# Kernel tuning notes

Hardware: AMD Instinct MI355X
Metric: run time of the kernel (lower is better)

The kernel has to match this reference:

```python
import jax, jax.numpy as jnp
import numpy as np

WD, WH, WW = 7, 7, 7  # 3D window size


def _relative_position_index():
    # Matches the torch buffer construction exactly.
    coords = np.stack(np.meshgrid(np.arange(WD), np.arange(WH), np.arange(WW), indexing='ij'))  # [3,wd,wh,ww]
    cf = coords.reshape(3, -1)                      # [3, n]
    rel = cf[:, :, None] - cf[:, None, :]           # [3, n, n]
    rel = rel.transpose(1, 2, 0).copy()             # [n, n, 3]
    rel[..., 0] += WD - 1
    rel[..., 1] += WH - 1
    rel[..., 2] += WW - 1
    rel[..., 0] *= (2 * WH - 1) * (2 * WW - 1)
    rel[..., 1] *= (2 * WW - 1)
    return rel.sum(-1).astype(np.int32)             # [n, n] in [0, 2197)


def setup_inputs() -> dict:
    key = jax.random.key(0)
    ks = jax.random.split(key, 10)
    DIM, H = 192, 6
    B, N, NW = 256, WD * WH * WW, 64  # b = batch*num_windows, NW divides B
    TABLE = (2 * WD - 1) * (2 * WH - 1) * (2 * WW - 1)  # 2197
    w_std = 0.02
    mask = jnp.where(jax.random.uniform(ks[2], (NW, N, N)) < 0.1, -100.0, 0.0).astype(jnp.float32)
    return {
        'x_q': jax.random.normal(ks[0], (B, N, DIM), jnp.float32),
        'x_kv': jax.random.normal(ks[1], (B, N, DIM), jnp.float32),
        'mask': mask,
        'q_w': jax.random.normal(ks[3], (DIM, DIM), jnp.float32) * w_std,
        'q_b': jnp.zeros((DIM,), jnp.float32),
        'kv_w': jax.random.normal(ks[4], (2 * DIM, DIM), jnp.float32) * w_std,
        'kv_b': jnp.zeros((2 * DIM,), jnp.float32),
        'proj_w': jax.random.normal(ks[5], (DIM, DIM), jnp.float32) * w_std,
        'proj_b': jnp.zeros((DIM,), jnp.float32),
        'rpb_table': jax.random.normal(ks[6], (TABLE, H), jnp.float32) * w_std,
        'rpi': jnp.asarray(_relative_position_index()),
    }


def reference(x_q, x_kv, mask, q_w, q_b, kv_w, kv_b, proj_w, proj_b, rpb_table, rpi):
    b, n, c = x_q.shape
    h = rpb_table.shape[-1]
    d = c // h
    scale = d ** (-0.5)
    # projections (torch Linear: y = x @ W.T + b)
    q = (x_q @ q_w.T + q_b).reshape(b, n, h, d)
    kv = x_kv @ kv_w.T + kv_b                      # [b, n, 2c]
    k = kv[..., :c].reshape(b, n, h, d)
    v = kv[..., c:].reshape(b, n, h, d)
    # windowed QK^T
    attn = jnp.einsum('bnhd,bmhd->bhnm', q * scale, k)  # [b, h, n, n]
    # gathered relative-position bias
    rpb = rpb_table[rpi[:n, :n].reshape(-1)].reshape(n, n, h).transpose(2, 0, 1)  # [h, n, n]
    attn = attn + rpb[None]
    # window mask add
    nw = mask.shape[0]
    attn = attn.reshape(b // nw, nw, h, n, n) + mask[None, :, None]
    attn = jax.nn.softmax(attn.reshape(b, h, n, n), axis=-1)
    out = jnp.einsum('bhnm,bmhd->bnhd', attn, v).reshape(b, n, c)
    return out @ proj_w.T + proj_b
```

## Files before the change

### kernel.cpp

```cpp
#include <hip/hip_runtime.h>
#include <hip/hip_bf16.h>
#include <cstdint>

#define B_    256
#define N_    343
#define C_    192
#define H_    6
#define D_    32
#define NW_   64
#define M_    (B_*N_)
#define NN_   (N_*N_)
#define VTS_  352
#define VLS_  360
#define RPG_  86
#define SCALE_ 0.17677669529663687f
#define LOG2E_ 1.4426950408889634f
#define SCALE_LOG2E_ (SCALE_ * LOG2E_)

typedef unsigned short ushort_t;
typedef __attribute__((ext_vector_type(8))) short short8;
typedef __attribute__((ext_vector_type(4))) float f32x4;
typedef __attribute__((ext_vector_type(16))) float f32x16;

__device__ __forceinline__ float b2f(unsigned int u) {
    return __uint_as_float(u << 16);
}
__device__ __forceinline__ unsigned int f2b(float f) {
    unsigned int x = __float_as_uint(f);
    x += 0x7FFFu + ((x >> 16) & 1u);
    return x >> 16;
}
__device__ __forceinline__ unsigned int cvt_pk(float a, float b) {
    unsigned int r;
    asm("v_cvt_pk_bf16_f32 %0, %1, %2" : "=v"(r) : "v"(a), "v"(b));
    return r;
}
__device__ __forceinline__ void pswap(unsigned int &x, unsigned int &y) {
    asm("v_permlane32_swap_b32 %0, %1" : "+v"(x), "+v"(y));
}

__global__ __launch_bounds__(256) void wcvt(
    const float* __restrict__ qw, const float* __restrict__ kvw,
    const float* __restrict__ pw, ushort_t* __restrict__ wb)
{
    int i = blockIdx.x * 256 + threadIdx.x;
    if (i >= 36864) return;
    float4 v;
    if (i < 9216)       v = ((const float4*)qw)[i];
    else if (i < 27648) v = ((const float4*)kvw)[i - 9216];
    else                v = ((const float4*)pw)[i - 27648];
    uint2 u;
    u.x = cvt_pk(v.x, v.y);
    u.y = cvt_pk(v.z, v.w);
    ((uint2*)wb)[i] = u;
}

__global__ __launch_bounds__(512, 4) void gemm_qkv(
    const float* __restrict__ xq, const float* __restrict__ xkv,
    const ushort_t* __restrict__ wb,
    const float* __restrict__ qbias, const float* __restrict__ kvbias,
    ushort_t* __restrict__ qx, ushort_t* __restrict__ kx,
    ushort_t* __restrict__ vtb)
{
    __shared__ ushort_t wls[192 * 200];

    const int t = threadIdx.x, wv = t >> 6, lane = t & 63;
    const int quad = lane >> 4, col = lane & 15;
    const int lid = blockIdx.x;
    const int xcd = lid & 7, idx = lid >> 3;
    const int wg = (xcd < 2 ? xcd * 258 : 2 * 258 + (xcd - 2) * 257) + idx;
    const int jsel = wg % 3;
    const int m0 = (wg / 3) * 128;
    const ushort_t* W = wb + (size_t)jsel * 36864;
    const float* Xf = (jsel == 0) ? xq : xkv;
    const float* bias = (jsel == 0) ? qbias : (jsel == 1 ? kvbias : kvbias + 192);
    const float alpha = (jsel == 0) ? SCALE_LOG2E_ : 1.0f;

    float4 a0[6], a1[6];
    {
        const float* xp = Xf + (size_t)(m0 + wv * 16 + col) * 192;
        #pragma unroll
        for (int kt = 0; kt < 6; ++kt) {
            a0[kt] = *(const float4*)(xp + kt * 32 + quad * 8);
            a1[kt] = *(const float4*)(xp + kt * 32 + quad * 8 + 4);
        }
    }

    for (int c = t; c < 4608; c += 512) {
        int row = c / 24, off = (c % 24) * 8;
        *(short8*)(wls + row * 200 + off) = *(const short8*)(W + row * 192 + off);
    }

    short8 xf[6];
    #pragma unroll
    for (int kt = 0; kt < 6; ++kt) {
        union { short8 s; unsigned int u[4]; } f;
        f.u[0] = cvt_pk(a0[kt].x, a0[kt].y);
        f.u[1] = cvt_pk(a0[kt].z, a0[kt].w);
        f.u[2] = cvt_pk(a1[kt].x, a1[kt].y);
        f.u[3] = cvt_pk(a1[kt].z, a1[kt].w);
        xf[kt] = f.s;
    }
    __syncthreads();

    f32x4 acc[12] = {};
    #pragma unroll
    for (int kt = 0; kt < 6; ++kt)
        #pragma unroll
        for (int ct = 0; ct < 12; ++ct) {
            short8 wf = *(const short8*)(wls + (ct * 16 + col) * 200 + kt * 32 + quad * 8);
            acc[ct] = __builtin_amdgcn_mfma_f32_16x16x32_bf16(wf, xf[kt], acc[ct], 0, 0, 0);
        }

    if (jsel < 2) {
        ushort_t* o16 = (jsel == 0) ? qx : kx;
        int m = m0 + wv * 16 + col;
        int bb = m / N_, nn = m - bb * N_;
        #pragma unroll
        for (int ct = 0; ct < 12; ++ct) {
            float4 bv = *(const float4*)(bias + ct * 16 + quad * 4);
            int hh = ct >> 1;
            int dbase = (ct & 1) * 16 + quad * 4;
            float v0 = (acc[ct][0] + bv.x) * alpha;
            float v1 = (acc[ct][1] + bv.y) * alpha;
            float v2 = (acc[ct][2] + bv.z) * alpha;
            float v3 = (acc[ct][3] + bv.w) * alpha;
            uint2 pk;
            pk.x = cvt_pk(v0, v1);
            pk.y = cvt_pk(v2, v3);
            *(uint2*)(o16 + (((size_t)bb * H_ + hh) * N_ + nn) * D_ + dbase) = pk;
        }
    } else {
        int m = m0 + wv * 16 + col;
        int bb = m / N_, nn = m - bb * N_;
        #pragma unroll
        for (int ct = 0; ct < 12; ++ct) {
            float4 bv = *(const float4*)(bias + ct * 16 + quad * 4);
            int hh = ct >> 1;
            int d0 = (ct & 1) * 16 + quad * 4;
            unsigned int u01 = cvt_pk(acc[ct][0] + bv.x, acc[ct][1] + bv.y);
            unsigned int u23 = cvt_pk(acc[ct][2] + bv.z, acc[ct][3] + bv.w);
            ushort_t* vp = vtb + (((size_t)bb * H_ + hh) * D_ + d0) * VTS_ + nn;
            vp[0]            = (ushort_t)u01;
            vp[VTS_]         = (ushort_t)(u01 >> 16);
            vp[2 * VTS_]     = (ushort_t)u23;
            vp[3 * VTS_]     = (ushort_t)(u23 >> 16);
        }
    }
}

__global__ __launch_bounds__(512, 4) void gemm_out(
    const ushort_t* __restrict__ aob, const ushort_t* __restrict__ wb,
    const float* __restrict__ pbias, float* __restrict__ out)
{
    __shared__ ushort_t wls[192 * 200];

    const int t = threadIdx.x, wv = t >> 6, lane = t & 63;
    const int quad = lane >> 4, col = lane & 15;
    const int m0 = blockIdx.x * 128;
    const ushort_t* W = wb + (size_t)3 * 36864;

    short8 xf[6];
    {
        const ushort_t* xp = aob + (size_t)(m0 + wv * 16 + col) * 192;
        #pragma unroll
        for (int kt = 0; kt < 6; ++kt)
            xf[kt] = *(const short8*)(xp + kt * 32 + quad * 8);
    }
    for (int c = t; c < 4608; c += 512) {
        int row = c / 24, off = (c % 24) * 8;
        *(short8*)(wls + row * 200 + off) = *(const short8*)(W + row * 192 + off);
    }
    __syncthreads();

    f32x4 acc[12] = {};
    #pragma unroll
    for (int kt = 0; kt < 6; ++kt)
        #pragma unroll
        for (int ct = 0; ct < 12; ++ct) {
            short8 wf = *(const short8*)(wls + (ct * 16 + col) * 200 + kt * 32 + quad * 8);
            acc[ct] = __builtin_amdgcn_mfma_f32_16x16x32_bf16(wf, xf[kt], acc[ct], 0, 0, 0);
        }

    int m = m0 + wv * 16 + col;
    #pragma unroll
    for (int ct = 0; ct < 12; ++ct) {
        float4 bv = *(const float4*)(pbias + ct * 16 + quad * 4);
        float4 vo;
        vo.x = acc[ct][0] + bv.x; vo.y = acc[ct][1] + bv.y;
        vo.z = acc[ct][2] + bv.z; vo.w = acc[ct][3] + bv.w;
        *(float4*)(out + (size_t)m * 192 + ct * 16 + quad * 4) = vo;
    }
}

__global__ __launch_bounds__(256) void rpb_gather_b(
    const float* __restrict__ table, const int* __restrict__ rpi,
    ushort_t* __restrict__ rpbt)
{
    int n = blockIdx.x;
    for (int m = threadIdx.x; m < N_; m += 256) {
        int id = rpi[n * N_ + m];
        int mg = m >> 2, mi = m & 3;
        #pragma unroll
        for (int h = 0; h < H_; ++h)
            rpbt[((((size_t)h * RPG_ + mg) * N_) + n) * 4 + mi] =
                (ushort_t)f2b(table[(size_t)id * H_ + h] * LOG2E_);
    }
}

__global__ __launch_bounds__(256) void mask_bits(
    const float* __restrict__ mask, unsigned int* __restrict__ mbt)
{
    int gw   = blockIdx.x * 4 + (threadIdx.x >> 6);
    int lane = threadIdx.x & 63;
    int n = gw % N_, w = gw / N_;
    if (w >= NW_) return;
    const float* mrow = mask + ((size_t)w * N_ + n) * N_;
    #pragma unroll
    for (int seg = 0; seg < 6; ++seg) {
        int m = seg * 64 + lane;
        float v = (m < N_) ? mrow[m] : -100.f;
        unsigned long long bm = __ballot(v > -50.f);
        if (lane < 2)
            mbt[((size_t)w * 12 + seg * 2 + lane) * N_ + n] =
                (unsigned int)(bm >> (lane * 32));
    }
}

__global__ __launch_bounds__(256) void vt_pad(ushort_t* __restrict__ vtb)
{
    int bh = blockIdx.x;
    for (int i = threadIdx.x; i < D_ * (VTS_ - N_); i += 256) {
        int d = i / (VTS_ - N_), m = N_ + i % (VTS_ - N_);
        vtb[((size_t)bh * D_ + d) * VTS_ + m] = 0;
    }
}

__global__ __launch_bounds__(256, 3) void attn_mfma(
    const ushort_t* __restrict__ qb, const ushort_t* __restrict__ kb,
    const ushort_t* __restrict__ vtb, const ushort_t* __restrict__ rpbt,
    const unsigned int* __restrict__ mbt, ushort_t* __restrict__ aob)
{
    __shared__ ushort_t ks[352 * 40];
    __shared__ ushort_t vls[32 * VLS_];

    const int t = threadIdx.x, wv = t >> 6, lane = t & 63;
    const int hh = lane >> 5, c = lane & 31;
    const int lid = blockIdx.x;
    const int wg = (lid & 7) * 576 + (lid >> 3);
    const int qt = wg % 3;
    const int bhx = wg / 3;
    const int h = bhx % H_, b = bhx / H_;
    const int bh = b * H_ + h;
    const int w  = b & (NW_ - 1);
    const int n0 = qt * 128 + wv * 32;

    const ushort_t* kbase = kb + (size_t)bh * (N_ * D_);
    for (int cc = t; cc < (N_ * D_) / 8; cc += 256) {
        int row = cc >> 2, off = (cc & 3) * 8;
        *(short8*)(ks + row * 40 + off) = *(const short8*)(kbase + cc * 8);
    }
    const ushort_t* vbase = vtb + (size_t)bh * (D_ * VTS_);
    for (int cc = t; cc < (D_ * VTS_) / 8; cc += 256) {
        int row = cc / 44, off = (cc % 44) * 8;
        *(short8*)(vls + row * VLS_ + off) = *(const short8*)(vbase + cc * 8);
    }

    int nn = n0 + c; if (nn > N_ - 1) nn = N_ - 1;
    const ushort_t* qp = qb + ((size_t)bh * N_ + nn) * D_;
    short8 qf0 = *(const short8*)(qp + hh * 8);
    short8 qf1 = *(const short8*)(qp + 16 + hh * 8);

    unsigned int dwv[12];
    {
        const unsigned int* mbp = mbt + (size_t)w * 12 * N_ + nn;
        #pragma unroll
        for (int i = 0; i < 12; ++i) dwv[i] = mbp[i * N_];
    }
    const uint2* rp2 = (const uint2*)rpbt + (size_t)h * (RPG_ * N_) + nn;

    __syncthreads();

    f32x16 oacc = {};
    float sum = 0.f;

    #pragma unroll
    for (int kt = 0; kt < 11; ++kt) {
        const ushort_t* krow = ks + (kt * 32 + c) * 40 + hh * 8;
        short8 ka  = *(const short8*)(krow);
        short8 kb2 = *(const short8*)(krow + 16);
        f32x16 s = {};
        s = __builtin_amdgcn_mfma_f32_32x32x16_bf16(ka,  qf0, s, 0, 0, 0);
        s = __builtin_amdgcn_mfma_f32_32x32x16_bf16(kb2, qf1, s, 0, 0, 0);

        unsigned int nibs = dwv[kt] >> (hh * 4);
        unsigned int pk[8];
        #pragma unroll
        for (int g = 0; g < 4; ++g) {
            int mg = kt * 8 + 2 * g + hh;
            if (mg > RPG_ - 1) mg = RPG_ - 1;
            uint2 rv = rp2[(size_t)mg * N_];
            unsigned int nib = (nibs >> (g * 8)) & 0xFu;
            float e0 = __builtin_exp2f(s[4*g+0] + b2f(rv.x & 0xffffu));
            float e1 = __builtin_exp2f(s[4*g+1] + b2f(rv.x >> 16));
            float e2 = __builtin_exp2f(s[4*g+2] + b2f(rv.y & 0xffffu));
            float e3 = __builtin_exp2f(s[4*g+3] + b2f(rv.y >> 16));
            e0 = (nib & 1u) ? e0 : 0.f;
            e1 = (nib & 2u) ? e1 : 0.f;
            e2 = (nib & 4u) ? e2 : 0.f;
            e3 = (nib & 8u) ? e3 : 0.f;
            sum += (e0 + e1) + (e2 + e3);
            pk[2*g]   = cvt_pk(e0, e1);
            pk[2*g+1] = cvt_pk(e2, e3);
        }
        pswap(pk[0], pk[2]);
        pswap(pk[1], pk[3]);
        pswap(pk[4], pk[6]);
        pswap(pk[5], pk[7]);
        union { short8 s8; unsigned int u[4]; } pf1, pf2;
        pf1.u[0] = pk[0]; pf1.u[1] = pk[1]; pf1.u[2] = pk[2]; pf1.u[3] = pk[3];
        pf2.u[0] = pk[4]; pf2.u[1] = pk[5]; pf2.u[2] = pk[6]; pf2.u[3] = pk[7];

        const ushort_t* vrow = vls + c * VLS_ + kt * 32 + hh * 8;
        short8 vf1 = *(const short8*)(vrow);
        short8 vf2 = *(const short8*)(vrow + 16);
        oacc = __builtin_amdgcn_mfma_f32_32x32x16_bf16(vf1, pf1.s8, oacc, 0, 0, 0);
        oacc = __builtin_amdgcn_mfma_f32_32x32x16_bf16(vf2, pf2.s8, oacc, 0, 0, 0);
    }

    sum += __shfl_xor(sum, 32);

    int n = n0 + c;
    if (n < N_) {
        float inv = 1.0f / sum;
        ushort_t* op = aob + ((size_t)b * N_ + n) * C_ + h * D_ + hh * 4;
        #pragma unroll
        for (int g = 0; g < 4; ++g) {
            uint2 pkk;
            pkk.x = cvt_pk(oacc[4*g+0] * inv, oacc[4*g+1] * inv);
            pkk.y = cvt_pk(oacc[4*g+2] * inv, oacc[4*g+3] * inv);
            *(uint2*)(op + g * 8) = pkk;
        }
    }
}

extern "C" void kernel_launch(void* const* d_in, const int* in_sizes, int n_in,
                              void* d_out, int out_size, void* d_ws, size_t ws_size,
                              hipStream_t stream)
{
    const float* x_q    = (const float*)d_in[0];
    const float* x_kv   = (const float*)d_in[1];
    const float* mask   = (const float*)d_in[2];
    const float* q_w    = (const float*)d_in[3];
    const float* q_b    = (const float*)d_in[4];
    const float* kv_w   = (const float*)d_in[5];
    const float* kv_b   = (const float*)d_in[6];
    const float* proj_w = (const float*)d_in[7];
    const float* proj_b = (const float*)d_in[8];
    const float* rpb_t  = (const float*)d_in[9];
    const int*   rpi    = (const int*)d_in[10];
    float* out = (float*)d_out;

    const size_t QKV  = (size_t)B_ * H_ * N_ * D_;
    const size_t QKV2 = (size_t)B_ * H_ * D_ * VTS_;
    char* ws = (char*)d_ws;
    ushort_t* qx   = (ushort_t*)ws;
    ushort_t* kx   = qx + QKV;
    ushort_t* vtb  = kx + QKV;
    ushort_t* aob  = vtb + QKV2;
    ushort_t* rpbt = aob + QKV;
    ushort_t* wb   = rpbt + (size_t)H_ * RPG_ * N_ * 4;
    unsigned int* mbt = (unsigned int*)(wb + 147456);

    wcvt<<<144, 256, 0, stream>>>(q_w, kv_w, proj_w, wb);
    rpb_gather_b<<<N_, 256, 0, stream>>>(rpb_t, rpi, rpbt);
    mask_bits<<<(NW_ * N_) / 4, 256, 0, stream>>>(mask, mbt);
    vt_pad<<<B_ * H_, 256, 0, stream>>>(vtb);
    gemm_qkv<<<2058, 512, 0, stream>>>(
        x_q, x_kv, wb, q_b, kv_b, qx, kx, vtb);
    attn_mfma<<<4608, 256, 0, stream>>>(qx, kx, vtb, rpbt, mbt, aob);
    gemm_out<<<M_/128, 512, 0, stream>>>(aob, wb, proj_b, out);
}
```

Before: 383.1 us.

## Double row tile per wave and persist gemm_qkv blocks over multiple jobs

Both projection GEMMs now give each wave 32 rows (two 16-row sub-tiles) instead of 16, so every weight fragment read from LDS feeds two MFMAs. gemm_qkv becomes a persistent kernel of 512 blocks, each handling 2 or 3 (row-group, weight) jobs, reloading weights and bias into LDS per job. Bias is staged in LDS. The trade-off is more registers and lower occupancy (launch bounds 512,2), fewer blocks to spread across CUs, and an extra barrier between jobs.

```diff
diff --git a/kernel.cpp b/kernel.cpp
--- a/kernel.cpp
+++ b/kernel.cpp
@@ -55,7 +55,7 @@
     ((uint2*)wb)[i] = u;
 }
 
-__global__ __launch_bounds__(512, 4) void gemm_qkv(
+__global__ __launch_bounds__(512, 2) void gemm_qkv(
     const float* __restrict__ xq, const float* __restrict__ xkv,
     const ushort_t* __restrict__ wb,
     const float* __restrict__ qbias, const float* __restrict__ kvbias,
@@ -63,133 +63,154 @@
     ushort_t* __restrict__ vtb)
 {
     __shared__ ushort_t wls[192 * 200];
+    __shared__ float    bls[192];
 
     const int t = threadIdx.x, wv = t >> 6, lane = t & 63;
     const int quad = lane >> 4, col = lane & 15;
-    const int lid = blockIdx.x;
-    const int xcd = lid & 7, idx = lid >> 3;
-    const int wg = (xcd < 2 ? xcd * 258 : 2 * 258 + (xcd - 2) * 257) + idx;
-    const int jsel = wg % 3;
-    const int m0 = (wg / 3) * 128;
-    const ushort_t* W = wb + (size_t)jsel * 36864;
-    const float* Xf = (jsel == 0) ? xq : xkv;
-    const float* bias = (jsel == 0) ? qbias : (jsel == 1 ? kvbias : kvbias + 192);
-    const float alpha = (jsel == 0) ? SCALE_LOG2E_ : 1.0f;
-
-    float4 a0[6], a1[6];
-    {
-        const float* xp = Xf + (size_t)(m0 + wv * 16 + col) * 192;
-        #pragma unroll
-        for (int kt = 0; kt < 6; ++kt) {
-            a0[kt] = *(const float4*)(xp + kt * 32 + quad * 8);
-            a1[kt] = *(const float4*)(xp + kt * 32 + quad * 8 + 4);
-        }
-    }
-
+    const int lbid = (blockIdx.x & 7) * 64 + (blockIdx.x >> 3);
+    const int start = lbid * 2 + (lbid < 5 ? lbid : 5);
+    const int cnt = 2 + (lbid < 5 ? 1 : 0);
+
+    for (int ji = 0; ji < cnt; ++ji) {
+        const int job = start + ji;
+        const int mgrp = job / 3, jsel = job - mgrp * 3;
+        const int m0 = mgrp * 256;
+        const float* Xf = (jsel == 0) ? xq : xkv;
+        const float* bias = (jsel == 0) ? qbias : (jsel == 1 ? kvbias : kvbias + 192);
+        const float alpha = (jsel == 0) ? SCALE_LOG2E_ : 1.0f;
+
+        if (ji) __syncthreads();
+        {
+            const ushort_t* W = wb + (size_t)jsel * 36864;
+            for (int c = t; c < 4608; c += 512) {
+                int row = c / 24, off = (c % 24) * 8;
+                *(short8*)(wls + row * 200 + off) = *(const short8*)(W + row * 192 + off);
+            }
+            if (t < 48) ((float4*)bls)[t] = ((const float4*)bias)[t];
+        }
+
+        short8 xf[2][6];
+        #pragma unroll
+        for (int sub = 0; sub < 2; ++sub) {
+            const float* xp = Xf + (size_t)(m0 + wv * 32 + sub * 16 + col) * 192;
+            float4 a0[6], a1[6];
+            #pragma unroll
+            for (int kt = 0; kt < 6; ++kt) {
+                a0[kt] = *(const float4*)(xp + kt * 32 + quad * 8);
+                a1[kt] = *(const float4*)(xp + kt * 32 + quad * 8 + 4);
+            }
+            #pragma unroll
+            for (int kt = 0; kt < 6; ++kt) {
+                union { short8 s; unsigned int u[4]; } f;
+                f.u[0] = cvt_pk(a0[kt].x, a0[kt].y);
+                f.u[1] = cvt_pk(a0[kt].z, a0[kt].w);
+                f.u[2] = cvt_pk(a1[kt].x, a1[kt].y);
+                f.u[3] = cvt_pk(a1[kt].z, a1[kt].w);
+                xf[sub][kt] = f.s;
+            }
+        }
+        __syncthreads();
+
+        f32x4 acc[2][12] = {};
+        #pragma unroll
+        for (int kt = 0; kt < 6; ++kt)
+            #pragma unroll
+            for (int ct = 0; ct < 12; ++ct) {
+                short8 wf = *(const short8*)(wls + (ct * 16 + col) * 200 + kt * 32 + quad * 8);
+                acc[0][ct] = __builtin_amdgcn_mfma_f32_16x16x32_bf16(wf, xf[0][kt], acc[0][ct], 0, 0, 0);
+                acc[1][ct] = __builtin_amdgcn_mfma_f32_16x16x32_bf16(wf, xf[1][kt], acc[1][ct], 0, 0, 0);
+            }
+
+        if (jsel < 2) {
+            ushort_t* o16 = (jsel == 0) ? qx : kx;
+            #pragma unroll
+            for (int sub = 0; sub < 2; ++sub) {
+                int m = m0 + wv * 32 + sub * 16 + col;
+                int bb = m / N_, nn = m - bb * N_;
+                #pragma unroll
+                for (int ct = 0; ct < 12; ++ct) {
+                    float4 bv = *(const float4*)(bls + ct * 16 + quad * 4);
+                    int hh = ct >> 1;
+                    int dbase = (ct & 1) * 16 + quad * 4;
+                    float v0 = (acc[sub][ct][0] + bv.x) * alpha;
+                    float v1 = (acc[sub][ct][1] + bv.y) * alpha;
+                    float v2 = (acc[sub][ct][2] + bv.z) * alpha;
+                    float v3 = (acc[sub][ct][3] + bv.w) * alpha;
+                    uint2 pk;
+                    pk.x = cvt_pk(v0, v1);
+                    pk.y = cvt_pk(v2, v3);
+                    *(uint2*)(o16 + (((size_t)bb * H_ + hh) * N_ + nn) * D_ + dbase) = pk;
+                }
+            }
+        } else {
+            #pragma unroll
+            for (int sub = 0; sub < 2; ++sub) {
+                int m = m0 + wv * 32 + sub * 16 + col;
+                int bb = m / N_, nn = m - bb * N_;
+                #pragma unroll
+                for (int ct = 0; ct < 12; ++ct) {
+                    float4 bv = *(const float4*)(bls + ct * 16 + quad * 4);
+                    int hh = ct >> 1;
+                    int d0 = (ct & 1) * 16 + quad * 4;
+                    unsigned int u01 = cvt_pk(acc[sub][ct][0] + bv.x, acc[sub][ct][1] + bv.y);
+                    unsigned int u23 = cvt_pk(acc[sub][ct][2] + bv.z, acc[sub][ct][3] + bv.w);
+                    ushort_t* vp = vtb + (((size_t)bb * H_ + hh) * D_ + d0) * VTS_ + nn;
+                    vp[0]            = (ushort_t)u01;
+                    vp[VTS_]         = (ushort_t)(u01 >> 16);
+                    vp[2 * VTS_]     = (ushort_t)u23;
+                    vp[3 * VTS_]     = (ushort_t)(u23 >> 16);
+                }
+            }
+        }
+    }
+}
+
+__global__ __launch_bounds__(512, 2) void gemm_out(
+    const ushort_t* __restrict__ aob, const ushort_t* __restrict__ wb,
+    const float* __restrict__ pbias, float* __restrict__ out)
+{
+    __shared__ ushort_t wls[192 * 200];
+
+    const int t = threadIdx.x, wv = t >> 6, lane = t & 63;
+    const int quad = lane >> 4, col = lane & 15;
+    const int m0 = blockIdx.x * 256;
+    const ushort_t* W = wb + (size_t)3 * 36864;
+
+    short8 xf[2][6];
+    #pragma unroll
+    for (int sub = 0; sub < 2; ++sub) {
+        const ushort_t* xp = aob + (size_t)(m0 + wv * 32 + sub * 16 + col) * 192;
+        #pragma unroll
+        for (int kt = 0; kt < 6; ++kt)
+            xf[sub][kt] = *(const short8*)(xp + kt * 32 + quad * 8);
+    }
     for (int c = t; c < 4608; c += 512) {
         int row = c / 24, off = (c % 24) * 8;
         *(short8*)(wls + row * 200 + off) = *(const short8*)(W + row * 192 + off);
     }
-
-    short8 xf[6];
-    #pragma unroll
-    for (int kt = 0; kt < 6; ++kt) {
-        union { short8 s; unsigned int u[4]; } f;
-        f.u[0] = cvt_pk(a0[kt].x, a0[kt].y);
-        f.u[1] = cvt_pk(a0[kt].z, a0[kt].w);
-        f.u[2] = cvt_pk(a1[kt].x, a1[kt].y);
-        f.u[3] = cvt_pk(a1[kt].z, a1[kt].w);
-        xf[kt] = f.s;
-    }
     __syncthreads();
 
-    f32x4 acc[12] = {};
+    f32x4 acc[2][12] = {};
     #pragma unroll
     for (int kt = 0; kt < 6; ++kt)
         #pragma unroll
         for (int ct = 0; ct < 12; ++ct) {
             short8 wf = *(const short8*)(wls + (ct * 16 + col) * 200 + kt * 32 + quad * 8);
-            acc[ct] = __builtin_amdgcn_mfma_f32_16x16x32_bf16(wf, xf[kt], acc[ct], 0, 0, 0);
-        }
-
-    if (jsel < 2) {
-        ushort_t* o16 = (jsel == 0) ? qx : kx;
-        int m = m0 + wv * 16 + col;
-        int bb = m / N_, nn = m - bb * N_;
+            acc[0][ct] = __builtin_amdgcn_mfma_f32_16x16x32_bf16(wf, xf[0][kt], acc[0][ct], 0, 0, 0);
+            acc[1][ct] = __builtin_amdgcn_mfma_f32_16x16x32_bf16(wf, xf[1][kt], acc[1][ct], 0, 0, 0);
+        }
+
+    #pragma unroll
+    for (int sub = 0; sub < 2; ++sub) {
+        int m = m0 + wv * 32 + sub * 16 + col;
         #pragma unroll
         for (int ct = 0; ct < 12; ++ct) {
-            float4 bv = *(const float4*)(bias + ct * 16 + quad * 4);
-            int hh = ct >> 1;
-            int dbase = (ct & 1) * 16 + quad * 4;
-            float v0 = (acc[ct][0] + bv.x) * alpha;
-            float v1 = (acc[ct][1] + bv.y) * alpha;
-            float v2 = (acc[ct][2] + bv.z) * alpha;
-            float v3 = (acc[ct][3] + bv.w) * alpha;
-            uint2 pk;
-            pk.x = cvt_pk(v0, v1);
-            pk.y = cvt_pk(v2, v3);
-            *(uint2*)(o16 + (((size_t)bb * H_ + hh) * N_ + nn) * D_ + dbase) = pk;
-        }
-    } else {
-        int m = m0 + wv * 16 + col;
-        int bb = m / N_, nn = m - bb * N_;
-        #pragma unroll
-        for (int ct = 0; ct < 12; ++ct) {
-            float4 bv = *(const float4*)(bias + ct * 16 + quad * 4);
-            int hh = ct >> 1;
-            int d0 = (ct & 1) * 16 + quad * 4;
-            unsigned int u01 = cvt_pk(acc[ct][0] + bv.x, acc[ct][1] + bv.y);
-            unsigned int u23 = cvt_pk(acc[ct][2] + bv.z, acc[ct][3] + bv.w);
-            ushort_t* vp = vtb + (((size_t)bb * H_ + hh) * D_ + d0) * VTS_ + nn;
-            vp[0]            = (ushort_t)u01;
-            vp[VTS_]         = (ushort_t)(u01 >> 16);
-            vp[2 * VTS_]     = (ushort_t)u23;
-            vp[3 * VTS_]     = (ushort_t)(u23 >> 16);
-        }
-    }
-}
-
-__global__ __launch_bounds__(512, 4) void gemm_out(
-    const ushort_t* __restrict__ aob, const ushort_t* __restrict__ wb,
-    const float* __restrict__ pbias, float* __restrict__ out)
-{
-    __shared__ ushort_t wls[192 * 200];
-
-    const int t = threadIdx.x, wv = t >> 6, lane = t & 63;
-    const int quad = lane >> 4, col = lane & 15;
-    const int m0 = blockIdx.x * 128;
-    const ushort_t* W = wb + (size_t)3 * 36864;
-
-    short8 xf[6];
-    {
-        const ushort_t* xp = aob + (size_t)(m0 + wv * 16 + col) * 192;
-        #pragma unroll
-        for (int kt = 0; kt < 6; ++kt)
-            xf[kt] = *(const short8*)(xp + kt * 32 + quad * 8);
-    }
-    for (int c = t; c < 4608; c += 512) {
-        int row = c / 24, off = (c % 24) * 8;
-        *(short8*)(wls + row * 200 + off) = *(const short8*)(W + row * 192 + off);
-    }
-    __syncthreads();
-
-    f32x4 acc[12] = {};
-    #pragma unroll
-    for (int kt = 0; kt < 6; ++kt)
-        #pragma unroll
-        for (int ct = 0; ct < 12; ++ct) {
-            short8 wf = *(const short8*)(wls + (ct * 16 + col) * 200 + kt * 32 + quad * 8);
-            acc[ct] = __builtin_amdgcn_mfma_f32_16x16x32_bf16(wf, xf[kt], acc[ct], 0, 0, 0);
-        }
-
-    int m = m0 + wv * 16 + col;
-    #pragma unroll
-    for (int ct = 0; ct < 12; ++ct) {
-        float4 bv = *(const float4*)(pbias + ct * 16 + quad * 4);
-        float4 vo;
-        vo.x = acc[ct][0] + bv.x; vo.y = acc[ct][1] + bv.y;
-        vo.z = acc[ct][2] + bv.z; vo.w = acc[ct][3] + bv.w;
-        *(float4*)(out + (size_t)m * 192 + ct * 16 + quad * 4) = vo;
+            float4 bv = *(const float4*)(pbias + ct * 16 + quad * 4);
+            float4 vo;
+            vo.x = acc[sub][ct][0] + bv.x; vo.y = acc[sub][ct][1] + bv.y;
+            vo.z = acc[sub][ct][2] + bv.z; vo.w = acc[sub][ct][3] + bv.w;
+            *(float4*)(out + (size_t)m * 192 + ct * 16 + quad * 4) = vo;
+        }
     }
 }
 
@@ -376,8 +397,8 @@
     rpb_gather_b<<<N_, 256, 0, stream>>>(rpb_t, rpi, rpbt);
     mask_bits<<<(NW_ * N_) / 4, 256, 0, stream>>>(mask, mbt);
     vt_pad<<<B_ * H_, 256, 0, stream>>>(vtb);
-    gemm_qkv<<<2058, 512, 0, stream>>>(
+    gemm_qkv<<<512, 512, 0, stream>>>(
         x_q, x_kv, wb, q_b, kv_b, qx, kx, vtb);
     attn_mfma<<<4608, 256, 0, stream>>>(qx, kx, vtb, rpbt, mbt, aob);
-    gemm_out<<<M_/128, 512, 0, stream>>>(aob, wb, proj_b, out);
-}
+    gemm_out<<<343, 512, 0, stream>>>(aob, wb, proj_b, out);
+}
```

New measurement: 385.9 us. About the same (+0.7%).
